# Kernel optimization log

Hardware: AMD Instinct MI355X
Metric: run time of the kernel (lower is better)

The kernel has to match this reference:

```python
import jax, jax.numpy as jnp
import numpy as np
from math import sqrt

B, S, E, H = 4, 4096, 512, 64


def setup_inputs() -> dict:
    key = jax.random.key(0)
    ks = jax.random.split(key, 9)
    std = sqrt(2.0 / (E + 4 * H))
    x_query = jax.random.normal(ks[0], (B, S, E), dtype=jnp.float32)
    x_key = jax.random.normal(ks[1], (B, S, E), dtype=jnp.float32)
    x_value = jax.random.normal(ks[2], (B, S, E), dtype=jnp.float32)
    Wq = jax.random.normal(ks[3], (E, H), dtype=jnp.float32) * std
    Wk = jax.random.normal(ks[4], (E, H), dtype=jnp.float32) * std
    Wv = jax.random.normal(ks[5], (E, H), dtype=jnp.float32) * std
    bq = jnp.zeros((H,), dtype=jnp.float32)
    bk = jnp.zeros((H,), dtype=jnp.float32)
    bv = jnp.zeros((H,), dtype=jnp.float32)
    # causal mask: True entries are masked out (set to -inf), as in scores[mask] = -inf
    mask = jnp.broadcast_to(jnp.triu(jnp.ones((S, S), dtype=bool), k=1), (B, S, S))
    return {"x_query": x_query, "x_key": x_key, "x_value": x_value,
            "Wq": Wq, "bq": bq, "Wk": Wk, "bk": bk, "Wv": Wv, "bv": bv,
            "mask": mask}


def reference(x_query, x_key, x_value, Wq, bq, Wk, bk, Wv, bv, mask):
    scale = 1.0 / sqrt(H)
    Q = x_query @ Wq + bq              # [B, S, H]
    K = x_key @ Wk + bk                # [B, S, H]
    V = x_value @ Wv + bv              # [B, S, H]
    scores = jnp.einsum('bqh,bkh->bqk', Q, K) * scale  # [B, S, S]
    scores = jnp.where(mask, -jnp.inf, scores)
    attn = jax.nn.softmax(scores, axis=-1)
    Z = jnp.einsum('bqk,bkh->bqh', attn, V)             # [B, S, H]
    return Z
```

## Files before the change

kernel.cpp:

```cpp
#include <hip/hip_runtime.h>
#include <math.h>

#define BB 4
#define SS 4096
#define EE 512
#define HH 64
#define NSPLIT 8
#define NQ (BB * SS)

typedef _Float16 f16x8 __attribute__((ext_vector_type(8)));
typedef short    s16x8 __attribute__((ext_vector_type(8)));
typedef float    f32x4 __attribute__((ext_vector_type(4)));

static __device__ __forceinline__ unsigned short f2h(float f) {
    _Float16 h = (_Float16)f;
    return __builtin_bit_cast(unsigned short, h);
}

static __device__ __forceinline__ f32x4 mfma_f16(s16x8 a, s16x8 b, f32x4 c) {
    return __builtin_amdgcn_mfma_f32_16x16x32_f16(
        __builtin_bit_cast(f16x8, a), __builtin_bit_cast(f16x8, b), c, 0, 0, 0);
}

__global__ __launch_bounds__(256) void wprep_kernel(
    const float* __restrict__ Wq, const float* __restrict__ Wk,
    const float* __restrict__ Wv, unsigned short* __restrict__ WT)
{
    const int mat = blockIdx.y;
    const float* W = (mat == 0) ? Wq : ((mat == 1) ? Wk : Wv);
    const int base = blockIdx.x * 2048;
    for (int ii = threadIdx.x; ii < 2048; ii += 256) {
        const int i = base + ii;
        const int k = i >> 6, n = i & 63;
        WT[((size_t)mat * HH + n) * EE + k] = f2h(W[i]);
    }
}

__global__ __launch_bounds__(256) void qkv_proj_kernel(
    const float* __restrict__ Xq, const float* __restrict__ Xk, const float* __restrict__ Xv,
    const float* __restrict__ bq, const float* __restrict__ bk, const float* __restrict__ bv,
    const unsigned short* __restrict__ WT,
    unsigned short* __restrict__ Qf, unsigned short* __restrict__ Kf,
    unsigned short* __restrict__ Vt)
{
    const int mtx = blockIdx.y;
    const float* X    = (mtx == 0) ? Xq : ((mtx == 1) ? Xk : Xv);
    const float* bias = (mtx == 0) ? bq : ((mtx == 1) ? bk : bv);

    __shared__ unsigned short As[64 * 72];
    __shared__ unsigned short Bs[64 * 72];

    const int tid  = threadIdx.x;
    const int lane = tid & 63;
    const int w    = tid >> 6;
    const int l15  = lane & 15;
    const int lg   = lane >> 4;
    const int r0   = blockIdx.x * 64;

    const int arow = tid >> 2;
    const int asg  = tid & 3;

    f32x4 acc[4] = {{0,0,0,0},{0,0,0,0},{0,0,0,0},{0,0,0,0}};

    for (int c = 0; c < EE / 64; ++c) {
        const float* xp = &X[(size_t)(r0 + arow) * EE + c * 64 + asg * 16];
        const float4 x0 = ((const float4*)xp)[0];
        const float4 x1 = ((const float4*)xp)[1];
        const float4 x2 = ((const float4*)xp)[2];
        const float4 x3 = ((const float4*)xp)[3];
        const size_t wb = ((size_t)mtx * HH + arow) * EE + c * 64 + asg * 16;
        const s16x8 w0 = *(const s16x8*)&WT[wb];
        const s16x8 w1 = *(const s16x8*)&WT[wb + 8];
        __syncthreads();

        const float xs[16] = {x0.x,x0.y,x0.z,x0.w, x1.x,x1.y,x1.z,x1.w,
                              x2.x,x2.y,x2.z,x2.w, x3.x,x3.y,x3.z,x3.w};
        s16x8 a0, a1;
        #pragma unroll
        for (int i = 0; i < 8; ++i) {
            a0[i] = (short)f2h(xs[i]);
            a1[i] = (short)f2h(xs[8 + i]);
        }
        *(s16x8*)&As[arow * 72 + asg * 16]     = a0;
        *(s16x8*)&As[arow * 72 + asg * 16 + 8] = a1;
        *(s16x8*)&Bs[arow * 72 + asg * 16]     = w0;
        *(s16x8*)&Bs[arow * 72 + asg * 16 + 8] = w1;
        __syncthreads();

        const int ma = (w * 16 + l15) * 72;
        const s16x8 af0 = *(const s16x8*)&As[ma + lg * 8];
        const s16x8 af1 = *(const s16x8*)&As[ma + 32 + lg * 8];
        #pragma unroll
        for (int f = 0; f < 4; ++f) {
            const int nb = (f * 16 + l15) * 72;
            const s16x8 bf0 = *(const s16x8*)&Bs[nb + lg * 8];
            const s16x8 bf1 = *(const s16x8*)&Bs[nb + 32 + lg * 8];
            acc[f] = mfma_f16(af0, bf0, acc[f]);
            acc[f] = mfma_f16(af1, bf1, acc[f]);
        }
    }

    float bcol[4];
    #pragma unroll
    for (int f = 0; f < 4; ++f) bcol[f] = bias[f * 16 + l15];
    const float qs = (mtx == 0) ? 0.125f : 1.0f;

    if (mtx < 2) {
        unsigned short* Out = (mtx == 0) ? Qf : Kf;
        #pragma unroll
        for (int f = 0; f < 4; ++f)
            #pragma unroll
            for (int r = 0; r < 4; ++r)
                Out[(size_t)(r0 + w * 16 + lg * 4 + r) * HH + f * 16 + l15] =
                    f2h((acc[f][r] + bcol[f]) * qs);
    } else {
        const int b  = r0 >> 12;
        const int s0 = (r0 & 4095) + w * 16 + lg * 4;
        #pragma unroll
        for (int f = 0; f < 4; ++f) {
            ushort4 pk;
            pk.x = f2h(acc[f][0] + bcol[f]);
            pk.y = f2h(acc[f][1] + bcol[f]);
            pk.z = f2h(acc[f][2] + bcol[f]);
            pk.w = f2h(acc[f][3] + bcol[f]);
            *(ushort4*)&Vt[((size_t)b * HH + f * 16 + l15) * SS + s0] = pk;
        }
    }
}

__global__ __launch_bounds__(256) void attn_partial_kernel(
    const unsigned short* __restrict__ Qf, const unsigned short* __restrict__ Kf,
    const unsigned short* __restrict__ Vt, float* __restrict__ o_part,
    float* __restrict__ m_part, float* __restrict__ l_part)
{
    __shared__ unsigned short Ks[2][64 * 68];
    __shared__ unsigned short Vs[2][64 * 68];
    __shared__ unsigned short Pl[4 * 16 * 68];

    const int tid  = threadIdx.x;
    const int b    = blockIdx.z;
    const int cch  = blockIdx.y;
    const int qb0  = blockIdx.x * 64;
    const int lane = tid & 63;
    const int w    = tid >> 6;
    const int l15  = lane & 15;
    const int lg   = lane >> 4;
    const int qw0  = qb0 + w * 16;

    const size_t qrow = (size_t)(b * SS + qw0 + l15) * HH;
    const s16x8 qf0 = *(const s16x8*)&Qf[qrow + lg * 8];
    const s16x8 qf1 = *(const s16x8*)&Qf[qrow + 32 + lg * 8];

    f32x4 o[4] = {{0,0,0,0},{0,0,0,0},{0,0,0,0},{0,0,0,0}};
    float m[4], l[4];
    #pragma unroll
    for (int r = 0; r < 4; ++r) { m[r] = -1.0e30f; l[r] = 0.f; }

    const int kkey = tid >> 2, ksg = tid & 3;
    const unsigned short* Kb = Kf + (size_t)b * SS * HH;
    const unsigned short* Vb = Vt + (size_t)b * HH * SS;

    const int T   = blockIdx.x + 1;
    const int tpc = (T + NSPLIT - 1) / NSPLIT;
    const int t0  = cch * tpc;
    const int t1  = min(t0 + tpc, T);
    const int nt  = t1 - t0;
    unsigned short* PW = Pl + w * (16 * 68);

    s16x8 ka, kb2, va, vb2;

    if (nt > 0) {
        const int k0 = t0 * 64;
        ka  = *(const s16x8*)&Kb[(size_t)(k0 + kkey) * HH + ksg * 8];
        kb2 = *(const s16x8*)&Kb[(size_t)(k0 + kkey) * HH + 32 + ksg * 8];
        va  = *(const s16x8*)&Vb[(size_t)kkey * SS + k0 + ksg * 8];
        vb2 = *(const s16x8*)&Vb[(size_t)kkey * SS + k0 + 32 + ksg * 8];
        *(s16x8*)&Ks[0][kkey * 68 + ksg * 8]      = ka;
        *(s16x8*)&Ks[0][kkey * 68 + 32 + ksg * 8] = kb2;
        *(s16x8*)&Vs[0][kkey * 68 + ksg * 8]      = va;
        *(s16x8*)&Vs[0][kkey * 68 + 32 + ksg * 8] = vb2;
        __syncthreads();
    }

    for (int i = 0; i < nt; ++i) {
        const int t   = t0 + i;
        const int cur = i & 1;
        const int k0  = t * 64;

        if (i + 1 < nt) {
            const int kn = (t + 1) * 64;
            ka  = *(const s16x8*)&Kb[(size_t)(kn + kkey) * HH + ksg * 8];
            kb2 = *(const s16x8*)&Kb[(size_t)(kn + kkey) * HH + 32 + ksg * 8];
            va  = *(const s16x8*)&Vb[(size_t)kkey * SS + kn + ksg * 8];
            vb2 = *(const s16x8*)&Vb[(size_t)kkey * SS + kn + 32 + ksg * 8];
        }

        f32x4 sc[4];
        #pragma unroll
        for (int f = 0; f < 4; ++f) {
            const int kr = (f * 16 + l15) * 68;
            const s16x8 kfa = *(const s16x8*)&Ks[cur][kr + lg * 8];
            const s16x8 kfb = *(const s16x8*)&Ks[cur][kr + 32 + lg * 8];
            f32x4 z = {0, 0, 0, 0};
            z = mfma_f16(qf0, kfa, z);
            z = mfma_f16(qf1, kfb, z);
            sc[f] = z;
        }

        float sv[4][4];
        #pragma unroll
        for (int f = 0; f < 4; ++f)
            #pragma unroll
            for (int r = 0; r < 4; ++r) sv[f][r] = sc[f][r];
        if (k0 + 63 > qw0) {
            #pragma unroll
            for (int f = 0; f < 4; ++f)
                #pragma unroll
                for (int r = 0; r < 4; ++r) {
                    const int qr = qw0 + lg * 4 + r;
                    if (k0 + f * 16 + l15 > qr) sv[f][r] = -3.0e38f;
                }
        }

        float tm[4];
        #pragma unroll
        for (int r = 0; r < 4; ++r)
            tm[r] = fmaxf(fmaxf(sv[0][r], sv[1][r]), fmaxf(sv[2][r], sv[3][r]));
        #pragma unroll
        for (int d = 1; d < 16; d <<= 1)
            #pragma unroll
            for (int r = 0; r < 4; ++r) tm[r] = fmaxf(tm[r], __shfl_xor(tm[r], d));

        bool grow = false;
        #pragma unroll
        for (int r = 0; r < 4; ++r) grow = grow || (tm[r] > m[r] + 8.0f);
        if (__any((int)grow)) {
            #pragma unroll
            for (int r = 0; r < 4; ++r) {
                const float mn = fmaxf(m[r], tm[r]);
                const float al = __expf(m[r] - mn);
                m[r] = mn;
                l[r] *= al;
                #pragma unroll
                for (int f = 0; f < 4; ++f) o[f][r] *= al;
            }
        }

        float p[4][4];
        #pragma unroll
        for (int f = 0; f < 4; ++f)
            #pragma unroll
            for (int r = 0; r < 4; ++r) p[f][r] = __expf(sv[f][r] - m[r]);
        #pragma unroll
        for (int r = 0; r < 4; ++r)
            l[r] += p[0][r] + p[1][r] + p[2][r] + p[3][r];

        #pragma unroll
        for (int f = 0; f < 4; ++f)
            #pragma unroll
            for (int r = 0; r < 4; ++r)
                PW[(lg * 4 + r) * 68 + f * 16 + l15] = f2h(p[f][r]);
        const s16x8 pa0 = *(const s16x8*)&PW[l15 * 68 + lg * 8];
        const s16x8 pa1 = *(const s16x8*)&PW[l15 * 68 + 32 + lg * 8];
        #pragma unroll
        for (int f = 0; f < 4; ++f) {
            const int vr = (f * 16 + l15) * 68;
            const s16x8 vfa = *(const s16x8*)&Vs[cur][vr + lg * 8];
            const s16x8 vfb = *(const s16x8*)&Vs[cur][vr + 32 + lg * 8];
            o[f] = mfma_f16(pa0, vfa, o[f]);
            o[f] = mfma_f16(pa1, vfb, o[f]);
        }

        if (i + 1 < nt) {
            const int nxt = cur ^ 1;
            *(s16x8*)&Ks[nxt][kkey * 68 + ksg * 8]      = ka;
            *(s16x8*)&Ks[nxt][kkey * 68 + 32 + ksg * 8] = kb2;
            *(s16x8*)&Vs[nxt][kkey * 68 + ksg * 8]      = va;
            *(s16x8*)&Vs[nxt][kkey * 68 + 32 + ksg * 8] = vb2;
            __syncthreads();
        }
    }

    #pragma unroll
    for (int d = 1; d < 16; d <<= 1)
        #pragma unroll
        for (int r = 0; r < 4; ++r) l[r] += __shfl_xor(l[r], d);

    #pragma unroll
    for (int r = 0; r < 4; ++r) {
        const size_t qlin = (size_t)b * SS + qb0 + w * 16 + lg * 4 + r;
        float* Op = o_part + ((size_t)cch * NQ + qlin) * HH;
        #pragma unroll
        for (int f = 0; f < 4; ++f) Op[f * 16 + l15] = o[f][r];
        if (l15 == 0) {
            m_part[(size_t)cch * NQ + qlin] = m[r];
            l_part[(size_t)cch * NQ + qlin] = l[r];
        }
    }
}

__global__ __launch_bounds__(256) void attn_combine_kernel(
    const float* __restrict__ o_part, const float* __restrict__ m_part,
    const float* __restrict__ l_part, float* __restrict__ O)
{
    const int g = blockIdx.x * 256 + threadIdx.x;
    const size_t qlin = (size_t)(g >> 4);
    const int h0 = (g & 15) * 4;

    float mv[NSPLIT], lv[NSPLIT];
    float M = -INFINITY;
    #pragma unroll
    for (int cc = 0; cc < NSPLIT; ++cc) {
        mv[cc] = m_part[(size_t)cc * NQ + qlin];
        lv[cc] = l_part[(size_t)cc * NQ + qlin];
        M = fmaxf(M, mv[cc]);
    }
    float L = 0.f;
    float4 acc = make_float4(0.f, 0.f, 0.f, 0.f);
    #pragma unroll
    for (int cc = 0; cc < NSPLIT; ++cc) {
        const float wc = __expf(mv[cc] - M);
        L += lv[cc] * wc;
        const float4 oc = *(const float4*)&o_part[((size_t)cc * NQ + qlin) * HH + h0];
        acc.x += wc * oc.x; acc.y += wc * oc.y;
        acc.z += wc * oc.z; acc.w += wc * oc.w;
    }
    const float inv = 1.0f / L;
    acc.x *= inv; acc.y *= inv; acc.z *= inv; acc.w *= inv;
    *(float4*)&O[qlin * HH + h0] = acc;
}

extern "C" void kernel_launch(void* const* d_in, const int* in_sizes, int n_in,
                              void* d_out, int out_size, void* d_ws, size_t ws_size,
                              hipStream_t stream) {
    const float* xq = (const float*)d_in[0];
    const float* xk = (const float*)d_in[1];
    const float* xv = (const float*)d_in[2];
    const float* Wq = (const float*)d_in[3];
    const float* bq = (const float*)d_in[4];
    const float* Wk = (const float*)d_in[5];
    const float* bk = (const float*)d_in[6];
    const float* Wv = (const float*)d_in[7];
    const float* bv = (const float*)d_in[8];

    unsigned short* Qf = (unsigned short*)d_ws;
    unsigned short* Kf = Qf + (size_t)NQ * HH;
    unsigned short* Vt = Kf + (size_t)NQ * HH;
    unsigned short* WT = Vt + (size_t)NQ * HH;
    float* o_part = (float*)(WT + (size_t)3 * HH * EE);
    float* m_part = o_part + (size_t)NSPLIT * NQ * HH;
    float* l_part = m_part + (size_t)NSPLIT * NQ;

    wprep_kernel<<<dim3(16, 3), 256, 0, stream>>>(Wq, Wk, Wv, WT);

    qkv_proj_kernel<<<dim3(NQ / 64, 3), 256, 0, stream>>>(
        xq, xk, xv, bq, bk, bv, WT, Qf, Kf, Vt);

    attn_partial_kernel<<<dim3(SS / 64, NSPLIT, BB), 256, 0, stream>>>(
        Qf, Kf, Vt, o_part, m_part, l_part);

    attn_combine_kernel<<<(NQ * 16) / 256, 256, 0, stream>>>(
        o_part, m_part, l_part, (float*)d_out);
}
```

Baseline: 439.7 us.

## Load MFMA operands directly from global memory, dropping LDS staging

Both the QKV projection and the attention partial kernel stop staging tiles in shared memory. Each wave now loads its MFMA fragments straight from global memory (X/W in the projection, K/V in attention), which removes the barriers, LDS writes and double buffering. In exchange, every wave reloads the same K/V tiles, relying on L1/L2 cache, and loses the software prefetch that overlapped the next tile's loads with compute.

```diff
diff --git a/kernel.cpp b/kernel.cpp
--- a/kernel.cpp
+++ b/kernel.cpp
@@ -47,56 +47,33 @@
     const float* X    = (mtx == 0) ? Xq : ((mtx == 1) ? Xk : Xv);
     const float* bias = (mtx == 0) ? bq : ((mtx == 1) ? bk : bv);
 
-    __shared__ unsigned short As[64 * 72];
-    __shared__ unsigned short Bs[64 * 72];
-
     const int tid  = threadIdx.x;
     const int lane = tid & 63;
     const int w    = tid >> 6;
     const int l15  = lane & 15;
     const int lg   = lane >> 4;
     const int r0   = blockIdx.x * 64;
-
-    const int arow = tid >> 2;
-    const int asg  = tid & 3;
+    const int row  = r0 + w * 16 + l15;
+
+    const float* Xr = &X[(size_t)row * EE];
+    const unsigned short* Wm = &WT[(size_t)mtx * HH * EE];
 
     f32x4 acc[4] = {{0,0,0,0},{0,0,0,0},{0,0,0,0},{0,0,0,0}};
 
-    for (int c = 0; c < EE / 64; ++c) {
-        const float* xp = &X[(size_t)(r0 + arow) * EE + c * 64 + asg * 16];
-        const float4 x0 = ((const float4*)xp)[0];
-        const float4 x1 = ((const float4*)xp)[1];
-        const float4 x2 = ((const float4*)xp)[2];
-        const float4 x3 = ((const float4*)xp)[3];
-        const size_t wb = ((size_t)mtx * HH + arow) * EE + c * 64 + asg * 16;
-        const s16x8 w0 = *(const s16x8*)&WT[wb];
-        const s16x8 w1 = *(const s16x8*)&WT[wb + 8];
-        __syncthreads();
-
-        const float xs[16] = {x0.x,x0.y,x0.z,x0.w, x1.x,x1.y,x1.z,x1.w,
-                              x2.x,x2.y,x2.z,x2.w, x3.x,x3.y,x3.z,x3.w};
-        s16x8 a0, a1;
-        #pragma unroll
-        for (int i = 0; i < 8; ++i) {
-            a0[i] = (short)f2h(xs[i]);
-            a1[i] = (short)f2h(xs[8 + i]);
-        }
-        *(s16x8*)&As[arow * 72 + asg * 16]     = a0;
-        *(s16x8*)&As[arow * 72 + asg * 16 + 8] = a1;
-        *(s16x8*)&Bs[arow * 72 + asg * 16]     = w0;
-        *(s16x8*)&Bs[arow * 72 + asg * 16 + 8] = w1;
-        __syncthreads();
-
-        const int ma = (w * 16 + l15) * 72;
-        const s16x8 af0 = *(const s16x8*)&As[ma + lg * 8];
-        const s16x8 af1 = *(const s16x8*)&As[ma + 32 + lg * 8];
+    #pragma unroll 4
+    for (int kk = 0; kk < EE / 32; ++kk) {
+        const int kb = kk * 32 + lg * 8;
+        const float4 xa = *(const float4*)&Xr[kb];
+        const float4 xb = *(const float4*)&Xr[kb + 4];
+        s16x8 a;
+        a[0] = (short)f2h(xa.x); a[1] = (short)f2h(xa.y);
+        a[2] = (short)f2h(xa.z); a[3] = (short)f2h(xa.w);
+        a[4] = (short)f2h(xb.x); a[5] = (short)f2h(xb.y);
+        a[6] = (short)f2h(xb.z); a[7] = (short)f2h(xb.w);
         #pragma unroll
         for (int f = 0; f < 4; ++f) {
-            const int nb = (f * 16 + l15) * 72;
-            const s16x8 bf0 = *(const s16x8*)&Bs[nb + lg * 8];
-            const s16x8 bf1 = *(const s16x8*)&Bs[nb + 32 + lg * 8];
-            acc[f] = mfma_f16(af0, bf0, acc[f]);
-            acc[f] = mfma_f16(af1, bf1, acc[f]);
+            const s16x8 b = *(const s16x8*)&Wm[(size_t)(f * 16 + l15) * EE + kb];
+            acc[f] = mfma_f16(a, b, acc[f]);
         }
     }
 
@@ -133,8 +110,6 @@
     const unsigned short* __restrict__ Vt, float* __restrict__ o_part,
     float* __restrict__ m_part, float* __restrict__ l_part)
 {
-    __shared__ unsigned short Ks[2][64 * 68];
-    __shared__ unsigned short Vs[2][64 * 68];
     __shared__ unsigned short Pl[4 * 16 * 68];
 
     const int tid  = threadIdx.x;
@@ -156,7 +131,6 @@
     #pragma unroll
     for (int r = 0; r < 4; ++r) { m[r] = -1.0e30f; l[r] = 0.f; }
 
-    const int kkey = tid >> 2, ksg = tid & 3;
     const unsigned short* Kb = Kf + (size_t)b * SS * HH;
     const unsigned short* Vb = Vt + (size_t)b * HH * SS;
 
@@ -164,43 +138,17 @@
     const int tpc = (T + NSPLIT - 1) / NSPLIT;
     const int t0  = cch * tpc;
     const int t1  = min(t0 + tpc, T);
-    const int nt  = t1 - t0;
     unsigned short* PW = Pl + w * (16 * 68);
 
-    s16x8 ka, kb2, va, vb2;
-
-    if (nt > 0) {
-        const int k0 = t0 * 64;
-        ka  = *(const s16x8*)&Kb[(size_t)(k0 + kkey) * HH + ksg * 8];
-        kb2 = *(const s16x8*)&Kb[(size_t)(k0 + kkey) * HH + 32 + ksg * 8];
-        va  = *(const s16x8*)&Vb[(size_t)kkey * SS + k0 + ksg * 8];
-        vb2 = *(const s16x8*)&Vb[(size_t)kkey * SS + k0 + 32 + ksg * 8];
-        *(s16x8*)&Ks[0][kkey * 68 + ksg * 8]      = ka;
-        *(s16x8*)&Ks[0][kkey * 68 + 32 + ksg * 8] = kb2;
-        *(s16x8*)&Vs[0][kkey * 68 + ksg * 8]      = va;
-        *(s16x8*)&Vs[0][kkey * 68 + 32 + ksg * 8] = vb2;
-        __syncthreads();
-    }
-
-    for (int i = 0; i < nt; ++i) {
-        const int t   = t0 + i;
-        const int cur = i & 1;
-        const int k0  = t * 64;
-
-        if (i + 1 < nt) {
-            const int kn = (t + 1) * 64;
-            ka  = *(const s16x8*)&Kb[(size_t)(kn + kkey) * HH + ksg * 8];
-            kb2 = *(const s16x8*)&Kb[(size_t)(kn + kkey) * HH + 32 + ksg * 8];
-            va  = *(const s16x8*)&Vb[(size_t)kkey * SS + kn + ksg * 8];
-            vb2 = *(const s16x8*)&Vb[(size_t)kkey * SS + kn + 32 + ksg * 8];
-        }
+    for (int t = t0; t < t1; ++t) {
+        const int k0 = t * 64;
 
         f32x4 sc[4];
         #pragma unroll
         for (int f = 0; f < 4; ++f) {
-            const int kr = (f * 16 + l15) * 68;
-            const s16x8 kfa = *(const s16x8*)&Ks[cur][kr + lg * 8];
-            const s16x8 kfb = *(const s16x8*)&Ks[cur][kr + 32 + lg * 8];
+            const unsigned short* kr = &Kb[(size_t)(k0 + f * 16 + l15) * HH + lg * 8];
+            const s16x8 kfa = *(const s16x8*)kr;
+            const s16x8 kfb = *(const s16x8*)(kr + 32);
             f32x4 z = {0, 0, 0, 0};
             z = mfma_f16(qf0, kfa, z);
             z = mfma_f16(qf1, kfb, z);
@@ -262,22 +210,14 @@
                 PW[(lg * 4 + r) * 68 + f * 16 + l15] = f2h(p[f][r]);
         const s16x8 pa0 = *(const s16x8*)&PW[l15 * 68 + lg * 8];
         const s16x8 pa1 = *(const s16x8*)&PW[l15 * 68 + 32 + lg * 8];
+
         #pragma unroll
         for (int f = 0; f < 4; ++f) {
-            const int vr = (f * 16 + l15) * 68;
-            const s16x8 vfa = *(const s16x8*)&Vs[cur][vr + lg * 8];
-            const s16x8 vfb = *(const s16x8*)&Vs[cur][vr + 32 + lg * 8];
+            const unsigned short* vr = &Vb[(size_t)(f * 16 + l15) * SS + k0 + lg * 8];
+            const s16x8 vfa = *(const s16x8*)vr;
+            const s16x8 vfb = *(const s16x8*)(vr + 32);
             o[f] = mfma_f16(pa0, vfa, o[f]);
             o[f] = mfma_f16(pa1, vfb, o[f]);
-        }
-
-        if (i + 1 < nt) {
-            const int nxt = cur ^ 1;
-            *(s16x8*)&Ks[nxt][kkey * 68 + ksg * 8]      = ka;
-            *(s16x8*)&Ks[nxt][kkey * 68 + 32 + ksg * 8] = kb2;
-            *(s16x8*)&Vs[nxt][kkey * 68 + ksg * 8]      = va;
-            *(s16x8*)&Vs[nxt][kkey * 68 + 32 + ksg * 8] = vb2;
-            __syncthreads();
         }
     }
 
```

Result: slower. 495.0 us (+12.6%).
